# Performance work log

Hardware: AMD Instinct MI355X
Metric: run time of the kernel (lower is better)

## Reference

```python
import jax, jax.numpy as jnp
import numpy as np

B, L, D, H = 2, 2048, 768, 12
DH = D // H          # 64
DFF = 4 * D          # 3072
ALPHA = 0.25         # lorentz_alpha
BLEND = 0.5          # blend for FFN and MinkowskiLayerNorm (set via set_blend)
EPS = 1e-5
SCALE = float(np.sqrt(DH))


def setup_inputs() -> dict:
    key = jax.random.key(0)
    ks = jax.random.split(key, 14)
    w = lambda k, shape: jax.random.normal(k, shape, jnp.float32) * 0.02
    causal = jnp.tril(jnp.ones((L, L), bool))
    attention_mask = jnp.where(causal, 0.0, -1e9).astype(jnp.float32)[None, None]
    return {
        'x': jax.random.normal(ks[0], (B, L, D), jnp.float32),
        'attention_mask': attention_mask,
        'timelike_mask': jax.random.bernoulli(ks[1], 0.25, (D,)),
        'Wq': w(ks[2], (D, D)), 'Wk': w(ks[3], (D, D)),
        'Wv': w(ks[4], (D, D)), 'Wo': w(ks[5], (D, D)),
        'w1': w(ks[6], (DFF, D)), 'w2': w(ks[7], (D, DFF)),
        'w1_t': w(ks[8], (DFF // 2, D)), 'w2_t': w(ks[9], (D, DFF // 2)),
        'w1_s': w(ks[10], (DFF // 2, D)), 'w2_s': w(ks[11], (D, DFF // 2)),
        'n1_w': jnp.ones(D, jnp.float32), 'n1_b': jnp.zeros(D, jnp.float32),
        'n2_w': jnp.ones(D, jnp.float32), 'n2_b': jnp.zeros(D, jnp.float32),
    }


def _mink_norm(x, m, w, b):
    # Minkowski LayerNorm blended with standard LN (m: float timelike mask)
    mean = x.mean(-1, keepdims=True)
    xc = x - mean
    var = (xc * xc).mean(-1, keepdims=True)
    x_std = xc / jnp.sqrt(var + EPS)
    sq = xc * xc
    eta = (sq * (1.0 - m)).sum(-1, keepdims=True) - (sq * m).sum(-1, keepdims=True)
    x_eta = xc / jnp.sqrt(jnp.abs(eta) + EPS)
    xn = (1.0 - BLEND) * x_std + BLEND * x_eta
    return w * xn + b


def _attn(x, attention_mask, m, Wq, Wk, Wv, Wo):
    # (B,L,D) -> (B,H,L,DH)
    split = lambda t: t.reshape(B, L, H, DH).transpose(0, 2, 1, 3)
    Q = split(x @ Wq.T)
    K = split(x @ Wk.T)
    V = split(x @ Wv.T)
    scores = jnp.einsum('bhqd,bhkd->bhqk', Q, K) / SCALE
    # Minkowski timelike correction: per-head diagonal mask on Q
    m2 = m.reshape(H, DH)[None, :, None, :]          # (1,H,1,DH)
    Q_t = Q * m2
    q_norm = jnp.linalg.norm(Q, axis=-1, keepdims=True)
    qt_norm = jnp.linalg.norm(Q_t, axis=-1, keepdims=True)
    sf = jnp.where(qt_norm > 1e-6, q_norm / jnp.maximum(qt_norm, 1e-8), 0.0)
    time_inner = jnp.einsum('bhqd,bhkd->bhqk', Q_t * sf, K) / SCALE
    scores = scores - 2.0 * ALPHA * time_inner
    scores = scores + attention_mask
    aw = jax.nn.softmax(scores, axis=-1)
    out = jnp.einsum('bhqk,bhkd->bhqd', aw, V)
    out = out.transpose(0, 2, 1, 3).reshape(B, L, D)
    return out @ Wo.T


def _ffn(x, m, w1, w2, w1_t, w2_t, w1_s, w2_s):
    std_out = jax.nn.gelu(x @ w1.T, approximate=False) @ w2.T
    h_t = jax.nn.silu((x * m) @ w1_t.T) @ w2_t.T
    h_s = jax.nn.gelu((x * (1.0 - m)) @ w1_s.T, approximate=False) @ w2_s.T
    return (1.0 - BLEND) * std_out + BLEND * (h_t + h_s)


def reference(x, attention_mask, timelike_mask, Wq, Wk, Wv, Wo,
              w1, w2, w1_t, w2_t, w1_s, w2_s, n1_w, n1_b, n2_w, n2_b):
    m = timelike_mask.astype(jnp.float32)
    ao = _attn(_mink_norm(x, m, n1_w, n1_b), attention_mask, m, Wq, Wk, Wv, Wo)
    x = x + ao
    x = x + _ffn(_mink_norm(x, m, n2_w, n2_b), m, w1, w2, w1_t, w2_t, w1_s, w2_s)
    return x
```

## Files before the change

### kernel.cpp

```cpp
#include <hip/hip_runtime.h>


typedef unsigned short u16;
typedef __bf16 bfrag __attribute__((ext_vector_type(8)));
typedef float f32x4 __attribute__((ext_vector_type(4)));

#define MFMA(a, b, c) __builtin_amdgcn_mfma_f32_16x16x32_bf16(a, b, c, 0, 0, 0)
#define NEG_BIG (-30000.0f)
#define ASYNC16(g, l)                                                        \
  __builtin_amdgcn_global_load_lds(                                          \
      (const __attribute__((address_space(1))) unsigned int*)(g),            \
      (__attribute__((address_space(3))) unsigned int*)(l), 16, 0, 0)

__device__ __forceinline__ float bf2f(u16 u) {
  unsigned int v = ((unsigned int)u) << 16;
  float f; __builtin_memcpy(&f, &v, 4); return f;
}
__device__ __forceinline__ u16 f2bf(float f) {
  unsigned int v; __builtin_memcpy(&v, &f, 4);
  v += 0x7fffu + ((v >> 16) & 1u);
  return (u16)(v >> 16);
}
__device__ __forceinline__ bfrag ldfrag(const u16* p) {
  bfrag v; __builtin_memcpy(&v, p, 16); return v;
}

__global__ __launch_bounds__(256) void mask_conv_k(const void* __restrict__ mask,
                                                   float* __restrict__ mfl) {
  __shared__ int msh;
  if (threadIdx.x == 0) msh = 0;
  __syncthreads();
  const unsigned int* w = (const unsigned int*)mask;
  if (threadIdx.x < 192) {
    const unsigned int v = w[threadIdx.x];
    if ((v & 0xFFFFu) == 0x3F80u) atomicOr(&msh, 4);
    else if (v == 0x3F800000u) atomicOr(&msh, 2);
    else if (v >= 2u) atomicOr(&msh, 1);
  }
  __syncthreads();
  const int m = msh;
  const int mode = (m & 4) ? 3 : (m & 2) ? 2 : (m & 1) ? 1 : 0;
  for (int i = threadIdx.x; i < 768; i += 256) {
    int b;
    if (mode == 3) b = ((const u16*)mask)[i] != 0;
    else if (mode == 2) b = ((const float*)mask)[i] != 0.0f;
    else if (mode == 1) b = ((const unsigned char*)mask)[i] != 0;
    else b = ((const int*)mask)[i] != 0;
    mfl[i] = (float)b;
  }
}

struct Segs {
  const void* src[14];
  int off[14];
  int n[14];
  int mmode[14];
};

__global__ __launch_bounds__(256) void convert_k(Segs segs, u16* __restrict__ dstb,
                                                 const float* __restrict__ mfl) {
  const int seg = blockIdx.y;
  const int n = segs.n[seg];
  const int mm = segs.mmode[seg];
  u16* dst = dstb + segs.off[seg];
  const float* src = (const float*)segs.src[seg];
  for (int i = (blockIdx.x * 256 + threadIdx.x) * 4; i < n; i += gridDim.x * 1024) {
    float4 v;
    __builtin_memcpy(&v, src + i, 16);
    if (mm) {
      const int k = i % 768;
      float m0 = mfl[k], m1 = mfl[k + 1], m2 = mfl[k + 2], m3 = mfl[k + 3];
      if (mm == 2) { m0 = 1.f - m0; m1 = 1.f - m1; m2 = 1.f - m2; m3 = 1.f - m3; }
      v.x *= m0; v.y *= m1; v.z *= m2; v.w *= m3;
    }
    dst[i] = f2bf(v.x); dst[i + 1] = f2bf(v.y);
    dst[i + 2] = f2bf(v.z); dst[i + 3] = f2bf(v.w);
  }
}

__global__ __launch_bounds__(256) void mink_norm_k(
    const float* __restrict__ X, const float* __restrict__ mf,
    const u16* __restrict__ w, const u16* __restrict__ bias,
    u16* __restrict__ Y, float* __restrict__ Xcopy) {
  __shared__ float red[8];
  const int row = blockIdx.x, tid = threadIdx.x;
  const int wid = tid >> 6, lane = tid & 63;
  const size_t roff = (size_t)row * 768;

  float xv[3], mv[3];
  int idx[3];
#pragma unroll
  for (int i = 0; i < 3; i++) {
    idx[i] = tid + i * 256;
    xv[i] = X[roff + idx[i]];
    mv[i] = mf[idx[i]];
  }
  if (Xcopy) {
#pragma unroll
    for (int i = 0; i < 3; i++) Xcopy[roff + idx[i]] = xv[i];
  }
  float s = xv[0] + xv[1] + xv[2];
#pragma unroll
  for (int o = 32; o >= 1; o >>= 1) s += __shfl_xor(s, o, 64);
  if (lane == 0) red[wid] = s;
  __syncthreads();
  const float mean = (red[0] + red[1] + red[2] + red[3]) * (1.0f / 768.0f);
  __syncthreads();

  float xc[3], ss = 0.0f, sm = 0.0f;
#pragma unroll
  for (int i = 0; i < 3; i++) {
    xc[i] = xv[i] - mean;
    ss += xc[i] * xc[i];
    sm += xc[i] * xc[i] * mv[i];
  }
#pragma unroll
  for (int o = 32; o >= 1; o >>= 1) {
    ss += __shfl_xor(ss, o, 64);
    sm += __shfl_xor(sm, o, 64);
  }
  if (lane == 0) { red[wid] = ss; red[4 + wid] = sm; }
  __syncthreads();
  const float sumsq = red[0] + red[1] + red[2] + red[3];
  const float summ = red[4] + red[5] + red[6] + red[7];
  const float var = sumsq * (1.0f / 768.0f);
  const float eta = sumsq - 2.0f * summ;
  const float rs = 1.0f / sqrtf(var + 1e-5f);
  const float re = 1.0f / sqrtf(fabsf(eta) + 1e-5f);

#pragma unroll
  for (int i = 0; i < 3; i++) {
    const float xn = xc[i] * 0.5f * (rs + re);
    Y[roff + idx[i]] = f2bf(bf2f(w[idx[i]]) * xn + bf2f(bias[idx[i]]));
  }
}

__global__ __launch_bounds__(256) void qcorr_k(u16* __restrict__ Q,
                                               const float* __restrict__ mf) {
  const int idx = blockIdx.x * 4 + (threadIdx.x >> 6);
  const int t = threadIdx.x & 63;
  const int h = idx % 12;
  const int bl = idx / 12;
  const size_t off = (size_t)bl * 768 + h * 64 + t;
  const float q = bf2f(Q[off]);
  const float m = mf[h * 64 + t];
  float q2 = q * q, qm2 = q * q * m;
#pragma unroll
  for (int o = 32; o >= 1; o >>= 1) {
    q2 += __shfl_xor(q2, o, 64);
    qm2 += __shfl_xor(qm2, o, 64);
  }
  const float qn = sqrtf(q2), qtn = sqrtf(qm2);
  const float sf = (qtn > 1e-6f) ? qn / fmaxf(qtn, 1e-8f) : 0.0f;
  Q[off] = f2bf(q * (1.0f - 0.5f * sf * m) * 0.125f);
}

__device__ __forceinline__ void gemm128_loop(
    const u16* __restrict__ Ab, const u16* __restrict__ Wb2,
    int K, int lda, int ldb, u16 (*As)[32], u16 (*Bs)[32], f32x4 acc[4][4]) {
  const int tid = threadIdx.x;
  const int wid = tid >> 6, lane = tid & 63;
  const int lr = lane & 15, lq = lane >> 4;
  const int srow = wid * 32 + (lane >> 2);
  const int scol = (lane & 3) * 8;
  const u16* ga0 = Ab + (size_t)srow * lda + scol;
  const u16* ga1 = Ab + (size_t)(srow + 16) * lda + scol;
  const u16* gb0 = Wb2 + (size_t)srow * ldb + scol;
  const u16* gb1 = Wb2 + (size_t)(srow + 16) * ldb + scol;
  u16* la0 = &As[wid * 32][0];
  u16* la1 = &As[wid * 32 + 16][0];
  u16* lb0 = &Bs[wid * 32][0];
  u16* lb1 = &Bs[wid * 32 + 16][0];
  const int wr = (wid >> 1) * 64, wc = (wid & 1) * 64;

  for (int k0 = 0; k0 < K; k0 += 32) {
    __syncthreads();
    ASYNC16(ga0 + k0, la0);
    ASYNC16(ga1 + k0, la1);
    ASYNC16(gb0 + k0, lb0);
    ASYNC16(gb1 + k0, lb1);
    __syncthreads();
    bfrag af[4], bf4[4];
#pragma unroll
    for (int i = 0; i < 4; i++) af[i] = ldfrag(&As[wr + i * 16 + lr][lq * 8]);
#pragma unroll
    for (int j = 0; j < 4; j++) bf4[j] = ldfrag(&Bs[wc + j * 16 + lr][lq * 8]);
#pragma unroll
    for (int i = 0; i < 4; i++)
#pragma unroll
      for (int j = 0; j < 4; j++)
        acc[i][j] = MFMA(af[i], bf4[j], acc[i][j]);
  }
}

struct GSeg { const u16* W; u16* C; int ldc; int nblk; int epi; };
struct GArgs { GSeg s[3]; };

__global__ __launch_bounds__(256) void gemm128_fused(
    const u16* __restrict__ A, int lda, int K, GArgs args) {
  __shared__ __align__(16) u16 As[128][32];
  __shared__ __align__(16) u16 Bs[128][32];
  int cb = blockIdx.x, seg = 0;
  while (cb >= args.s[seg].nblk) { cb -= args.s[seg].nblk; seg++; }
  const GSeg g = args.s[seg];
  const int rowb = blockIdx.y * 128, colb = cb * 128;
  f32x4 acc[4][4] = {};
  gemm128_loop(A + (size_t)rowb * lda, g.W + (size_t)colb * K, K, lda, K,
               As, Bs, acc);

  const int lane = threadIdx.x & 63, wid = threadIdx.x >> 6;
  const int lr = lane & 15, lq = lane >> 4;
  const int wr = (wid >> 1) * 64, wc = (wid & 1) * 64;
#pragma unroll
  for (int i = 0; i < 4; i++)
#pragma unroll
    for (int j = 0; j < 4; j++)
#pragma unroll
      for (int r = 0; r < 4; r++) {
        const int row = rowb + wr + i * 16 + lq * 4 + r;
        const int col = colb + wc + j * 16 + lr;
        float v = acc[i][j][r];
        if (g.epi == 2) v = 0.5f * v * (1.0f + erff(v * 0.70710678118654752f));
        else if (g.epi == 3) v = v / (1.0f + __expf(-v));
        g.C[(size_t)row * g.ldc + col] = f2bf(v);
      }
}

__global__ __launch_bounds__(256) void gemm128_wo_splitk(
    const u16* __restrict__ A, const u16* __restrict__ W,
    float* __restrict__ Out) {
  __shared__ __align__(16) u16 As[128][32];
  __shared__ __align__(16) u16 Bs[128][32];
  const int rowb = blockIdx.y * 128, colb = blockIdx.x * 128;
  const int z = blockIdx.z;
  f32x4 acc[4][4] = {};
  gemm128_loop(A + (size_t)rowb * 768 + z * 384,
               W + (size_t)colb * 768 + z * 384, 384, 768, 768, As, Bs, acc);

  const int lane = threadIdx.x & 63, wid = threadIdx.x >> 6;
  const int lr = lane & 15, lq = lane >> 4;
  const int wr = (wid >> 1) * 64, wc = (wid & 1) * 64;
#pragma unroll
  for (int i = 0; i < 4; i++)
#pragma unroll
    for (int j = 0; j < 4; j++)
#pragma unroll
      for (int r = 0; r < 4; r++) {
        const int row = rowb + wr + i * 16 + lq * 4 + r;
        const int col = colb + wc + j * 16 + lr;
        atomicAdd(&Out[(size_t)row * 768 + col], acc[i][j][r]);
      }
}

__global__ __launch_bounds__(256) void ffn2_splitk(
    const u16* __restrict__ H1, const u16* __restrict__ Ht,
    const u16* __restrict__ Hs, const u16* __restrict__ W2,
    const u16* __restrict__ W2t, const u16* __restrict__ W2s,
    float* __restrict__ Out) {
  __shared__ __align__(16) u16 As[128][32];
  __shared__ __align__(16) u16 Bs[128][32];
  const int rowb = blockIdx.y * 128, colb = blockIdx.x * 128;
  const int z = blockIdx.z;
  f32x4 acc[4][4] = {};
  if (z == 0)
    gemm128_loop(H1 + (size_t)rowb * 3072, W2 + (size_t)colb * 3072,
                 1536, 3072, 3072, As, Bs, acc);
  else if (z == 1)
    gemm128_loop(H1 + (size_t)rowb * 3072 + 1536,
                 W2 + (size_t)colb * 3072 + 1536,
                 1536, 3072, 3072, As, Bs, acc);
  else if (z == 2)
    gemm128_loop(Ht + (size_t)rowb * 1536, W2t + (size_t)colb * 1536,
                 1536, 1536, 1536, As, Bs, acc);
  else
    gemm128_loop(Hs + (size_t)rowb * 1536, W2s + (size_t)colb * 1536,
                 1536, 1536, 1536, As, Bs, acc);

  const int lane = threadIdx.x & 63, wid = threadIdx.x >> 6;
  const int lr = lane & 15, lq = lane >> 4;
  const int wr = (wid >> 1) * 64, wc = (wid & 1) * 64;
#pragma unroll
  for (int i = 0; i < 4; i++)
#pragma unroll
    for (int j = 0; j < 4; j++)
#pragma unroll
      for (int r = 0; r < 4; r++) {
        const int row = rowb + wr + i * 16 + lq * 4 + r;
        const int col = colb + wc + j * 16 + lr;
        atomicAdd(&Out[(size_t)row * 768 + col], 0.5f * acc[i][j][r]);
      }
}

__global__ __launch_bounds__(256) void flash_attn_k(
    const u16* __restrict__ Qc, const u16* __restrict__ Kb,
    const u16* __restrict__ Vb, u16* __restrict__ O,
    float* __restrict__ Pn, float* __restrict__ Ph) {
  __shared__ __align__(16) u16 Ks[64][40];
  __shared__ __align__(16) u16 Vt[64][72];
  __shared__ __align__(16) u16 Ps[4][16][72];
  const int tid = threadIdx.x, wid = tid >> 6, lane = tid & 63;
  const int lr = lane & 15, lq = lane >> 4;

  int bx = blockIdx.x, qt = 0, c = 0;
  for (int q = 31; q >= 0; --q) {
    const int nc = (q < 8) ? 1 : (q / 8 + 1);
    if (bx < nc) { qt = q; c = bx; break; }
    bx -= nc;
  }
  const int nt = qt + 1;
  const int t0 = c * 8;
  const int t1 = (t0 + 8 < nt) ? t0 + 8 : nt;

  const int qb = qt * 64;
  const int bh = blockIdx.y;
  const int b = bh / 12, h = bh % 12;
  const int q0 = qb + wid * 16;
  const size_t base = (size_t)b * 2048 * 768 + h * 64;

  bfrag aq[2];
  aq[0] = ldfrag(Qc + base + (size_t)(q0 + lr) * 768 + lq * 8);
  aq[1] = ldfrag(Qc + base + (size_t)(q0 + lr) * 768 + 32 + lq * 8);

  f32x4 o[4] = {};
  float mrow[4] = {NEG_BIG, NEG_BIG, NEG_BIG, NEG_BIG};
  float lrow[4] = {0.0f, 0.0f, 0.0f, 0.0f};

  const int krow = tid >> 3;
  const int kcol = (tid & 7) * 8;
  const int vkey = tid & 31;
  const int vdg = tid >> 5;

  const u16* kp = Kb + base + (size_t)(t0 * 64 + krow) * 768 + kcol;
  const u16* vp = Vb + base + (size_t)(t0 * 64 + vkey) * 768 + vdg * 8;

  uint4 kv0, kv1, vv0, vv1;
  __builtin_memcpy(&kv0, kp, 16);
  __builtin_memcpy(&kv1, kp + (size_t)32 * 768, 16);
  __builtin_memcpy(&vv0, vp, 16);
  __builtin_memcpy(&vv1, vp + (size_t)32 * 768, 16);

  for (int kt = t0; kt < t1; kt++) {
    __syncthreads();
    __builtin_memcpy(&Ks[krow][kcol], &kv0, 16);
    __builtin_memcpy(&Ks[krow + 32][kcol], &kv1, 16);
    {
      union { uint4 u; u16 s[8]; } a, b2;
      a.u = vv0; b2.u = vv1;
#pragma unroll
      for (int j = 0; j < 8; j++) {
        Vt[vdg * 8 + j][vkey] = a.s[j];
        Vt[vdg * 8 + j][vkey + 32] = b2.s[j];
      }
    }
    __syncthreads();
    if (kt + 1 < t1) {
      const size_t koff = (size_t)(kt + 1 - t0) * 64 * 768;
      __builtin_memcpy(&kv0, kp + koff, 16);
      __builtin_memcpy(&kv1, kp + koff + (size_t)32 * 768, 16);
      __builtin_memcpy(&vv0, vp + koff, 16);
      __builtin_memcpy(&vv1, vp + koff + (size_t)32 * 768, 16);
    }

    const int kbk = kt * 64;
    {
      f32x4 s4[4] = {};
#pragma unroll
      for (int kg = 0; kg < 2; kg++) {
#pragma unroll
        for (int cc = 0; cc < 4; cc++) {
          bfrag bk = ldfrag(&Ks[cc * 16 + lr][kg * 32 + lq * 8]);
          s4[cc] = MFMA(aq[kg], bk, s4[cc]);
        }
      }
#pragma unroll
      for (int r = 0; r < 4; r++) {
        const int q = q0 + lq * 4 + r;
        float v[4];
        float mx = NEG_BIG;
#pragma unroll
        for (int cc = 0; cc < 4; cc++) {
          v[cc] = (kbk + cc * 16 + lr > q) ? NEG_BIG : s4[cc][r];
          mx = fmaxf(mx, v[cc]);
        }
#pragma unroll
        for (int off = 8; off >= 1; off >>= 1)
          mx = fmaxf(mx, __shfl_xor(mx, off, 16));
        const float mn = fmaxf(mrow[r], mx);
        const float alpha = __expf(mrow[r] - mn);
        float sm = 0.0f;
        float p[4];
#pragma unroll
        for (int cc = 0; cc < 4; cc++) {
          p[cc] = __expf(v[cc] - mn);
          sm += p[cc];
        }
#pragma unroll
        for (int off = 8; off >= 1; off >>= 1) sm += __shfl_xor(sm, off, 16);
        lrow[r] = lrow[r] * alpha + sm;
        mrow[r] = mn;
#pragma unroll
        for (int dt = 0; dt < 4; dt++) o[dt][r] *= alpha;
#pragma unroll
        for (int cc = 0; cc < 4; cc++)
          Ps[wid][lq * 4 + r][cc * 16 + lr] = f2bf(p[cc]);
      }
      __threadfence_block();
      bfrag pf0 = ldfrag(&Ps[wid][lr][lq * 8]);
      bfrag pf1 = ldfrag(&Ps[wid][lr][32 + lq * 8]);
#pragma unroll
      for (int dt = 0; dt < 4; dt++) {
        bfrag v0 = ldfrag(&Vt[dt * 16 + lr][lq * 8]);
        bfrag v1 = ldfrag(&Vt[dt * 16 + lr][32 + lq * 8]);
        o[dt] = MFMA(pf0, v0, o[dt]);
        o[dt] = MFMA(pf1, v1, o[dt]);
      }
    }
  }

  if (qt < 8) {
#pragma unroll
    for (int r = 0; r < 4; r++) {
      const float inv = 1.0f / fmaxf(lrow[r], 1e-30f);
      const int q = q0 + lq * 4 + r;
#pragma unroll
      for (int dt = 0; dt < 4; dt++)
        O[base + (size_t)q * 768 + dt * 16 + lr] = f2bf(o[dt][r] * inv);
    }
  } else {
    int off = 0;
    for (int j = 8; j < qt; ++j) off += j / 8 + 1;
    const int s = bh * 72 + off + c;
    float* Op = (s < 1536) ? Pn + (size_t)s * 4096
                           : Ph + (size_t)(s - 1536) * 4096;
    float* lmp = Ph + 786432 + (size_t)s * 128;
#pragma unroll
    for (int r = 0; r < 4; r++) {
      const int row = wid * 16 + lq * 4 + r;
#pragma unroll
      for (int dt = 0; dt < 4; dt++)
        Op[(size_t)row * 64 + dt * 16 + lr] = o[dt][r];
      if (lr == 0) { lmp[row] = mrow[r]; lmp[64 + row] = lrow[r]; }
    }
  }
}

__global__ __launch_bounds__(256) void attn_merge_k(
    const float* __restrict__ Pn, const float* __restrict__ Ph,
    u16* __restrict__ O) {
  const int qt = 8 + blockIdx.x;
  const int bh = blockIdx.y;
  const int b = bh / 12, h = bh % 12;
  const int nc = qt / 8 + 1;
  int off = 0;
  for (int j = 8; j < qt; ++j) off += j / 8 + 1;
  const int s0 = bh * 72 + off;
  const int row = threadIdx.x >> 2;
  const int c0 = (threadIdx.x & 3) * 16;
  const float* lmb = Ph + 786432;

  float mg = NEG_BIG;
  for (int cc = 0; cc < nc; ++cc)
    mg = fmaxf(mg, lmb[(size_t)(s0 + cc) * 128 + row]);

  float acc[16];
#pragma unroll
  for (int j = 0; j < 16; j++) acc[j] = 0.0f;
  float lg = 0.0f;
  for (int cc = 0; cc < nc; ++cc) {
    const int s = s0 + cc;
    const float mcv = lmb[(size_t)s * 128 + row];
    const float coef = __expf(mcv - mg);
    lg += coef * lmb[(size_t)s * 128 + 64 + row];
    const float* Op = (s < 1536) ? Pn + (size_t)s * 4096
                                 : Ph + (size_t)(s - 1536) * 4096;
    const float* rp = Op + (size_t)row * 64 + c0;
#pragma unroll
    for (int g = 0; g < 4; g++) {
      float4 v;
      __builtin_memcpy(&v, rp + g * 4, 16);
      acc[g * 4 + 0] += coef * v.x;
      acc[g * 4 + 1] += coef * v.y;
      acc[g * 4 + 2] += coef * v.z;
      acc[g * 4 + 3] += coef * v.w;
    }
  }
  const float inv = 1.0f / fmaxf(lg, 1e-30f);
  const int q = qt * 64 + row;
  const size_t ob = (size_t)b * 2048 * 768 + h * 64 + (size_t)q * 768 + c0;
#pragma unroll
  for (int j = 0; j < 16; j++) O[ob + j] = f2bf(acc[j] * inv);
}

extern "C" void kernel_launch(void* const* d_in, const int* in_sizes, int n_in,
                              void* d_out, int out_size, void* d_ws,
                              size_t ws_size, hipStream_t stream) {
  (void)in_sizes; (void)n_in; (void)out_size; (void)ws_size;
  const float* x = (const float*)d_in[0];
  const void* mask = d_in[2];

  char* ws = (char*)d_ws;
  u16* Wb  = (u16*)(ws);
  u16* n1h = (u16*)(ws + 23599104);
  u16* Qb  = (u16*)(ws + 48764928);
  u16* Kb2 = (u16*)(ws + 55056384);
  u16* Vb2 = (u16*)(ws + 61347840);
  u16* att = (u16*)(ws + 67639296);
  u16* hs  = (u16*)(ws + 80222208);
  float* mfl = (float*)(ws + 92805120);
  float* x1 = (float*)d_out;
  float* Pn = (float*)n1h;
  float* Ph = (float*)hs;

  u16* Wq = Wb + 0,        *Wk = Wb + 589824,   *Wv = Wb + 1179648;
  u16* Wo = Wb + 1769472,  *w1 = Wb + 2359296,  *w1t = Wb + 4718592;
  u16* w1s = Wb + 5898240, *w2 = Wb + 7077888,  *w2t = Wb + 9437184;
  u16* w2s = Wb + 10616832;
  u16* n1w = Wb + 11796480, *n1b = Wb + 11797248;
  u16* n2w = Wb + 11798016, *n2b = Wb + 11798784;

  Segs sg;
  const int srcidx[14] = {3, 4, 5, 6, 7, 9, 11, 8, 10, 12, 13, 14, 15, 16};
  const int offs[14] = {0, 589824, 1179648, 1769472, 2359296, 4718592,
                        5898240, 7077888, 9437184, 10616832,
                        11796480, 11797248, 11798016, 11798784};
  const int ns[14] = {589824, 589824, 589824, 589824, 2359296, 1179648,
                      1179648, 2359296, 1179648, 1179648, 768, 768, 768, 768};
  const int mms[14] = {0, 0, 0, 0, 0, 1, 2, 0, 0, 0, 0, 0, 0, 0};
  for (int i = 0; i < 14; i++) {
    sg.src[i] = d_in[srcidx[i]];
    sg.off[i] = offs[i];
    sg.n[i] = ns[i];
    sg.mmode[i] = mms[i];
  }

  mask_conv_k<<<1, 256, 0, stream>>>(mask, mfl);
  convert_k<<<dim3(2304, 14), 256, 0, stream>>>(sg, Wb, mfl);

  mink_norm_k<<<4096, 256, 0, stream>>>(x, mfl, n1w, n1b, n1h, x1);

  GArgs qkv;
  qkv.s[0] = {Wq, Qb, 768, 6, 0};
  qkv.s[1] = {Wk, Kb2, 768, 6, 0};
  qkv.s[2] = {Wv, Vb2, 768, 6, 0};
  gemm128_fused<<<dim3(18, 32), 256, 0, stream>>>(n1h, 768, 768, qkv);

  qcorr_k<<<12288, 256, 0, stream>>>(Qb, mfl);

  flash_attn_k<<<dim3(80, 24), 256, 0, stream>>>(Qb, Kb2, Vb2, att, Pn, Ph);
  attn_merge_k<<<dim3(24, 24), 256, 0, stream>>>(Pn, Ph, att);

  gemm128_wo_splitk<<<dim3(6, 32, 2), 256, 0, stream>>>(att, Wo, x1);

  mink_norm_k<<<4096, 256, 0, stream>>>(x1, mfl, n2w, n2b, Qb, nullptr);

  GArgs ffn1;
  ffn1.s[0] = {w1, n1h, 3072, 24, 2};
  ffn1.s[1] = {w1t, att, 1536, 12, 3};
  ffn1.s[2] = {w1s, hs, 1536, 12, 2};
  gemm128_fused<<<dim3(48, 32), 256, 0, stream>>>(Qb, 768, 768, ffn1);

  ffn2_splitk<<<dim3(6, 32, 4), 256, 0, stream>>>(n1h, att, hs, w2, w2t, w2s,
                                                  (float*)d_out);
}
```

Baseline: 444.7 us.

## Double-buffer LDS tiles in GEMM loop to overlap async loads with MFMA

The shared GEMM inner loop now uses two LDS buffers per operand. The next K-tile is issued with global_load_lds while the current tile is consumed by MFMAs, using explicit vmcnt waits and raw s_barrier calls in place of two full __syncthreads per step. This aims to hide global-memory latency in all three GEMM kernels (QKV/FFN1 fused, Wo split-K, FFN2 split-K). In exchange LDS use doubles to 32KB per block, which may lower occupancy, and correctness depends on the hand-set vmcnt counts.

```diff
diff --git a/kernel.cpp b/kernel.cpp
--- a/kernel.cpp
+++ b/kernel.cpp
@@ -167,30 +167,50 @@
   const u16* ga1 = Ab + (size_t)(srow + 16) * lda + scol;
   const u16* gb0 = Wb2 + (size_t)srow * ldb + scol;
   const u16* gb1 = Wb2 + (size_t)(srow + 16) * ldb + scol;
-  u16* la0 = &As[wid * 32][0];
-  u16* la1 = &As[wid * 32 + 16][0];
-  u16* lb0 = &Bs[wid * 32][0];
-  u16* lb1 = &Bs[wid * 32 + 16][0];
   const int wr = (wid >> 1) * 64, wc = (wid & 1) * 64;
-
-  for (int k0 = 0; k0 < K; k0 += 32) {
-    __syncthreads();
-    ASYNC16(ga0 + k0, la0);
-    ASYNC16(ga1 + k0, la1);
-    ASYNC16(gb0 + k0, lb0);
-    ASYNC16(gb1 + k0, lb1);
-    __syncthreads();
+  const int nt = K >> 5;
+
+#define STAGE16(dbuf, k0)                                                    \
+  {                                                                          \
+    u16* _a0 = &As[(dbuf) * 128 + wid * 32][0];                              \
+    u16* _a1 = &As[(dbuf) * 128 + wid * 32 + 16][0];                         \
+    u16* _b0 = &Bs[(dbuf) * 128 + wid * 32][0];                              \
+    u16* _b1 = &Bs[(dbuf) * 128 + wid * 32 + 16][0];                         \
+    ASYNC16(ga0 + (k0), _a0);                                                \
+    ASYNC16(ga1 + (k0), _a1);                                                \
+    ASYNC16(gb0 + (k0), _b0);                                                \
+    ASYNC16(gb1 + (k0), _b1);                                                \
+  }
+
+  STAGE16(0, 0);
+  for (int t = 0; t < nt; ++t) {
+    const int cur = t & 1;
+    if (t + 1 < nt) {
+      STAGE16(cur ^ 1, (t + 1) << 5);
+      __builtin_amdgcn_sched_barrier(0);
+      asm volatile("s_waitcnt vmcnt(4)" ::: "memory");
+    } else {
+      asm volatile("s_waitcnt vmcnt(0)" ::: "memory");
+    }
+    __builtin_amdgcn_s_barrier();
+    __builtin_amdgcn_sched_barrier(0);
     bfrag af[4], bf4[4];
 #pragma unroll
-    for (int i = 0; i < 4; i++) af[i] = ldfrag(&As[wr + i * 16 + lr][lq * 8]);
-#pragma unroll
-    for (int j = 0; j < 4; j++) bf4[j] = ldfrag(&Bs[wc + j * 16 + lr][lq * 8]);
+    for (int i = 0; i < 4; i++)
+      af[i] = ldfrag(&As[cur * 128 + wr + i * 16 + lr][lq * 8]);
+#pragma unroll
+    for (int j = 0; j < 4; j++)
+      bf4[j] = ldfrag(&Bs[cur * 128 + wc + j * 16 + lr][lq * 8]);
 #pragma unroll
     for (int i = 0; i < 4; i++)
 #pragma unroll
       for (int j = 0; j < 4; j++)
         acc[i][j] = MFMA(af[i], bf4[j], acc[i][j]);
-  }
+    asm volatile("s_waitcnt lgkmcnt(0)" ::: "memory");
+    __builtin_amdgcn_sched_barrier(0);
+    __builtin_amdgcn_s_barrier();
+  }
+#undef STAGE16
 }
 
 struct GSeg { const u16* W; u16* C; int ldc; int nblk; int epi; };
@@ -198,8 +218,8 @@
 
 __global__ __launch_bounds__(256) void gemm128_fused(
     const u16* __restrict__ A, int lda, int K, GArgs args) {
-  __shared__ __align__(16) u16 As[128][32];
-  __shared__ __align__(16) u16 Bs[128][32];
+  __shared__ __align__(16) u16 As[256][32];
+  __shared__ __align__(16) u16 Bs[256][32];
   int cb = blockIdx.x, seg = 0;
   while (cb >= args.s[seg].nblk) { cb -= args.s[seg].nblk; seg++; }
   const GSeg g = args.s[seg];
@@ -229,8 +249,8 @@
 __global__ __launch_bounds__(256) void gemm128_wo_splitk(
     const u16* __restrict__ A, const u16* __restrict__ W,
     float* __restrict__ Out) {
-  __shared__ __align__(16) u16 As[128][32];
-  __shared__ __align__(16) u16 Bs[128][32];
+  __shared__ __align__(16) u16 As[256][32];
+  __shared__ __align__(16) u16 Bs[256][32];
   const int rowb = blockIdx.y * 128, colb = blockIdx.x * 128;
   const int z = blockIdx.z;
   f32x4 acc[4][4] = {};
@@ -257,8 +277,8 @@
     const u16* __restrict__ Hs, const u16* __restrict__ W2,
     const u16* __restrict__ W2t, const u16* __restrict__ W2s,
     float* __restrict__ Out) {
-  __shared__ __align__(16) u16 As[128][32];
-  __shared__ __align__(16) u16 Bs[128][32];
+  __shared__ __align__(16) u16 As[256][32];
+  __shared__ __align__(16) u16 Bs[256][32];
   const int rowb = blockIdx.y * 128, colb = blockIdx.x * 128;
   const int z = blockIdx.z;
   f32x4 acc[4][4] = {};
```

Result: faster. 431.1 us (-3.1%).
